# Kernel optimization log

Measured on AMD Instinct MI355X. Metric: run time of the kernel, lower is better.

The kernel has to match this reference:

```python
import jax, jax.numpy as jnp
import numpy as np

TEMPERATURE = 0.5
EPS = 1e-8  # torch CosineSimilarity eps
# Per 4x4 chunk: mask excludes diag and k=+-2 -> negatives columns per row:
NEG_IDX = np.array([[1, 3], [0, 2], [1, 3], [0, 2]], dtype=np.int32)


def setup_inputs() -> dict:
    key = jax.random.key(0)
    k1, k2 = jax.random.split(key)
    zis = jax.random.normal(k1, (65536, 256), dtype=jnp.float32)
    zjs = jax.random.normal(k2, (65536, 256), dtype=jnp.float32)
    return {"zis": zis, "zjs": zjs}


def reference(zis, zjs):
    B, d = zis.shape
    n = B // 2  # number of chunks of size 2
    zi = zis.reshape(n, 2, d)
    zj = zjs.reshape(n, 2, d)
    reps = jnp.concatenate([zj, zi], axis=1)  # (n, 4, d) = [zjs_chunk, zis_chunk]
    # cosine similarity (normalize with eps like torch)
    norm = jnp.maximum(jnp.linalg.norm(reps, axis=-1, keepdims=True), EPS)
    reps_n = reps / norm
    sim = jnp.einsum('ncd,nkd->nck', reps_n, reps_n)  # (n, 4, 4)
    # positives: diag offsets +2 then -2 -> order [s02, s13, s20, s31]
    pos = jnp.stack([sim[:, 0, 2], sim[:, 1, 3], sim[:, 2, 0], sim[:, 3, 1]], axis=1)  # (n, 4)
    neg_idx = jnp.asarray(NEG_IDX)
    negs = jnp.take_along_axis(sim, neg_idx[None, :, :].astype(jnp.int32), axis=2)  # (n, 4, 2)
    logits = jnp.concatenate([pos[..., None], negs], axis=2) / TEMPERATURE  # (n, 4, 3)
    # CrossEntropy(reduction='sum') with label 0 per row
    loss = -jax.nn.log_softmax(logits, axis=-1)[..., 0]
    return jnp.sum(loss) / B  # original: total / (2 * batch_size) with batch_size=B... see notes
```

## Files before the change

### kernel.cpp

```cpp
#include <hip/hip_runtime.h>
#include <math.h>

#define D 256
#define EPS 1e-8f

__device__ __forceinline__ float row_loss(float pos, float na, float nb) {
    float l0 = pos + pos;
    float l1 = na + na;
    float l2 = nb + nb;
    float m  = fmaxf(l0, fmaxf(l1, l2));
    float e  = expf(l0 - m) + expf(l1 - m) + expf(l2 - m);
    return logf(e) - (l0 - m);
}

__global__ __launch_bounds__(256) void ntxent_partial_kernel(
    const float* __restrict__ zis, const float* __restrict__ zjs,
    int n_chunks, float* __restrict__ partial)
{
    const int tid      = blockIdx.x * 256 + threadIdx.x;
    const int lane8    = threadIdx.x & 7;
    const int group    = tid >> 3;
    const int n_groups = (gridDim.x * 256) >> 3;

    float local = 0.0f;

    for (int c = group; c < n_chunks; c += n_groups) {
        const float4* zi = (const float4*)(zis + (size_t)c * (2 * D));
        const float4* zj = (const float4*)(zjs + (size_t)c * (2 * D));

        float s00=0.f,s11=0.f,s22=0.f,s33=0.f;
        float s01=0.f,s02=0.f,s03=0.f,s12=0.f,s13=0.f,s23=0.f;
        #pragma unroll
        for (int j = 0; j < 8; ++j) {
            const int idx = lane8 + 8 * j;
            float4 r0 = zj[idx];
            float4 r1 = zj[64 + idx];
            float4 r2 = zi[idx];
            float4 r3 = zi[64 + idx];
            s00 += r0.x*r0.x + r0.y*r0.y + r0.z*r0.z + r0.w*r0.w;
            s11 += r1.x*r1.x + r1.y*r1.y + r1.z*r1.z + r1.w*r1.w;
            s22 += r2.x*r2.x + r2.y*r2.y + r2.z*r2.z + r2.w*r2.w;
            s33 += r3.x*r3.x + r3.y*r3.y + r3.z*r3.z + r3.w*r3.w;
            s01 += r0.x*r1.x + r0.y*r1.y + r0.z*r1.z + r0.w*r1.w;
            s02 += r0.x*r2.x + r0.y*r2.y + r0.z*r2.z + r0.w*r2.w;
            s03 += r0.x*r3.x + r0.y*r3.y + r0.z*r3.z + r0.w*r3.w;
            s12 += r1.x*r2.x + r1.y*r2.y + r1.z*r2.z + r1.w*r2.w;
            s13 += r1.x*r3.x + r1.y*r3.y + r1.z*r3.z + r1.w*r3.w;
            s23 += r2.x*r3.x + r2.y*r3.y + r2.z*r3.z + r2.w*r3.w;
        }

        #pragma unroll
        for (int m = 1; m < 8; m <<= 1) {
            s00 += __shfl_xor(s00, m);
            s11 += __shfl_xor(s11, m);
            s22 += __shfl_xor(s22, m);
            s33 += __shfl_xor(s33, m);
            s01 += __shfl_xor(s01, m);
            s02 += __shfl_xor(s02, m);
            s03 += __shfl_xor(s03, m);
            s12 += __shfl_xor(s12, m);
            s13 += __shfl_xor(s13, m);
            s23 += __shfl_xor(s23, m);
        }

        float rl = 0.0f;
        if (lane8 < 4) {
            const int r = lane8;
            float i0 = 1.0f / fmaxf(sqrtf(s00), EPS);
            float i1 = 1.0f / fmaxf(sqrtf(s11), EPS);
            float i2 = 1.0f / fmaxf(sqrtf(s22), EPS);
            float i3 = 1.0f / fmaxf(sqrtf(s33), EPS);
            float v01 = s01 * i0 * i1;
            float v02 = s02 * i0 * i2;
            float v03 = s03 * i0 * i3;
            float v12 = s12 * i1 * i2;
            float v13 = s13 * i1 * i3;
            float v23 = s23 * i2 * i3;
            float pos = (r & 1) ? v13 : v02;
            float na  = (r < 2) ? v01 : ((r == 2) ? v12 : v03);
            float nb  = (r == 0) ? v03 : ((r == 1) ? v12 : v23);
            rl = row_loss(pos, na, nb);
        }
        rl += __shfl_xor(rl, 1);
        rl += __shfl_xor(rl, 2);
        if (lane8 == 0) local += rl;
    }

    #pragma unroll
    for (int m = 1; m < 64; m <<= 1) local += __shfl_xor(local, m);
    __shared__ float red[4];
    if ((threadIdx.x & 63) == 0) red[threadIdx.x >> 6] = local;
    __syncthreads();
    if (threadIdx.x == 0) partial[blockIdx.x] = red[0] + red[1] + red[2] + red[3];
}

__global__ __launch_bounds__(256) void ntxent_final_kernel(
    const float* __restrict__ partial, int nb, float* __restrict__ out, float scale)
{
    float v = 0.0f;
    for (int i = threadIdx.x; i < nb; i += 256) v += partial[i];
    #pragma unroll
    for (int m = 1; m < 64; m <<= 1) v += __shfl_xor(v, m);
    __shared__ float red[4];
    if ((threadIdx.x & 63) == 0) red[threadIdx.x >> 6] = v;
    __syncthreads();
    if (threadIdx.x == 0) out[0] = (red[0] + red[1] + red[2] + red[3]) * scale;
}

extern "C" void kernel_launch(void* const* d_in, const int* in_sizes, int n_in,
                              void* d_out, int out_size, void* d_ws, size_t ws_size,
                              hipStream_t stream) {
    const float* zis = (const float*)d_in[0];
    const float* zjs = (const float*)d_in[1];
    float* out       = (float*)d_out;
    float* partial   = (float*)d_ws;

    const int B        = in_sizes[0] / D;
    const int n_chunks = B / 2;

    int nb = 1024;
    size_t cap = ws_size / sizeof(float);
    if (cap < (size_t)nb) nb = (int)(cap > 0 ? cap : 1);

    ntxent_partial_kernel<<<nb, 256, 0, stream>>>(zis, zjs, n_chunks, partial);
    ntxent_final_kernel<<<1, 256, 0, stream>>>(partial, nb, out, 1.0f / (float)B);
}
```

Baseline: 28.97 us.

## Map one chunk per 16-lane group with register prefetch and no grid-stride loop

Each chunk of four rows is now handled by a 16-lane group instead of an 8-lane group, and the persistent grid-stride loop is dropped. Instead the grid is sized so every group gets exactly one chunk, which means many more blocks. Inside the group, the next float4 batch is loaded into registers before the current one is accumulated, and the launch bounds request higher occupancy. The aim is more memory-level parallelism and less per-thread serial work on a bandwidth-bound reduction, at the cost of an extra shuffle stage and more partials for the final kernel. If the workspace is smaller than the block count, chunks would be silently skipped.

```diff
diff --git a/kernel.cpp b/kernel.cpp
--- a/kernel.cpp
+++ b/kernel.cpp
@@ -13,30 +13,38 @@
     return logf(e) - (l0 - m);
 }
 
-__global__ __launch_bounds__(256) void ntxent_partial_kernel(
+__global__ __launch_bounds__(256, 8) void ntxent_partial_kernel(
     const float* __restrict__ zis, const float* __restrict__ zjs,
     int n_chunks, float* __restrict__ partial)
 {
-    const int tid      = blockIdx.x * 256 + threadIdx.x;
-    const int lane8    = threadIdx.x & 7;
-    const int group    = tid >> 3;
-    const int n_groups = (gridDim.x * 256) >> 3;
+    const int tid   = blockIdx.x * 256 + threadIdx.x;
+    const int lane  = threadIdx.x & 15;
+    const int group = tid >> 4;
 
     float local = 0.0f;
 
-    for (int c = group; c < n_chunks; c += n_groups) {
-        const float4* zi = (const float4*)(zis + (size_t)c * (2 * D));
-        const float4* zj = (const float4*)(zjs + (size_t)c * (2 * D));
+    if (group < n_chunks) {
+        const float4* zi = (const float4*)(zis + (size_t)group * (2 * D));
+        const float4* zj = (const float4*)(zjs + (size_t)group * (2 * D));
 
         float s00=0.f,s11=0.f,s22=0.f,s33=0.f;
         float s01=0.f,s02=0.f,s03=0.f,s12=0.f,s13=0.f,s23=0.f;
+
+        float4 n0 = zj[lane];
+        float4 n1 = zj[64 + lane];
+        float4 n2 = zi[lane];
+        float4 n3 = zi[64 + lane];
+
         #pragma unroll
-        for (int j = 0; j < 8; ++j) {
-            const int idx = lane8 + 8 * j;
-            float4 r0 = zj[idx];
-            float4 r1 = zj[64 + idx];
-            float4 r2 = zi[idx];
-            float4 r3 = zi[64 + idx];
+        for (int i = 0; i < 4; ++i) {
+            float4 r0 = n0, r1 = n1, r2 = n2, r3 = n3;
+            if (i < 3) {
+                const int idx = lane + 16 * (i + 1);
+                n0 = zj[idx];
+                n1 = zj[64 + idx];
+                n2 = zi[idx];
+                n3 = zi[64 + idx];
+            }
             s00 += r0.x*r0.x + r0.y*r0.y + r0.z*r0.z + r0.w*r0.w;
             s11 += r1.x*r1.x + r1.y*r1.y + r1.z*r1.z + r1.w*r1.w;
             s22 += r2.x*r2.x + r2.y*r2.y + r2.z*r2.z + r2.w*r2.w;
@@ -50,7 +58,7 @@
         }
 
         #pragma unroll
-        for (int m = 1; m < 8; m <<= 1) {
+        for (int m = 1; m < 16; m <<= 1) {
             s00 += __shfl_xor(s00, m);
             s11 += __shfl_xor(s11, m);
             s22 += __shfl_xor(s22, m);
@@ -64,8 +72,8 @@
         }
 
         float rl = 0.0f;
-        if (lane8 < 4) {
-            const int r = lane8;
+        if (lane < 4) {
+            const int r = lane;
             float i0 = 1.0f / fmaxf(sqrtf(s00), EPS);
             float i1 = 1.0f / fmaxf(sqrtf(s11), EPS);
             float i2 = 1.0f / fmaxf(sqrtf(s22), EPS);
@@ -83,7 +91,7 @@
         }
         rl += __shfl_xor(rl, 1);
         rl += __shfl_xor(rl, 2);
-        if (lane8 == 0) local += rl;
+        if (lane == 0) local = rl;
     }
 
     #pragma unroll
@@ -118,7 +126,7 @@
     const int B        = in_sizes[0] / D;
     const int n_chunks = B / 2;
 
-    int nb = 1024;
+    int nb = (n_chunks * 16 + 255) / 256;
     size_t cap = ws_size / sizeof(float);
     if (cap < (size_t)nb) nb = (int)(cap > 0 ? cap : 1);
 
```

New measurement: 29.63 us. +2.3%, slower.
